# Optimization experiments

Measured on AMD Instinct MI355X. Metric: run time of the kernel, lower is better.

The kernel has to match this reference:

```python
import jax, jax.numpy as jnp
import numpy as np

B, Cin, Cout, T, H, W = 8, 64, 64, 16, 32, 32
AH = 64  # attention_hidden_dims


def setup_inputs() -> dict:
    key = jax.random.key(0)
    ks = jax.random.split(key, 6)
    s = 0.05
    return {
        "X": jax.random.normal(ks[0], (B, Cin, T, H, W), jnp.float32),
        # 1x1 conv weights of the SelfAttention module (bias zero-init like nn.Conv2d default is uniform, but zeros is fine for a reference baseline)
        "q_w": jax.random.normal(ks[1], (AH, Cin), jnp.float32) * s,
        "q_b": jnp.zeros((AH,), jnp.float32),
        "k_w": jax.random.normal(ks[2], (AH, Cin), jnp.float32) * s,
        "k_b": jnp.zeros((AH,), jnp.float32),
        "v_w": jax.random.normal(ks[3], (Cin, Cin), jnp.float32) * s,
        "v_b": jnp.zeros((Cin,), jnp.float32),
        # ConvLSTM gate conv: concat([x, h]) -> 4*Cout channels, 3x3, padding 1
        "conv_w": jax.random.normal(ks[4], (4 * Cout, Cin + Cout, 3, 3), jnp.float32) * s,
        "conv_b": jnp.zeros((4 * Cout,), jnp.float32),
        # peephole weights, zero-init per WeightsInitializer.Zeros
        "w_ci": jnp.zeros((Cout, H, W), jnp.float32),
        "w_cf": jnp.zeros((Cout, H, W), jnp.float32),
        "w_co": jnp.zeros((Cout, H, W), jnp.float32),
    }


def _self_attention(x, q_w, q_b, k_w, k_b, v_w, v_b):
    # x: (B, Cin, H, W). 1x1 convs expressed as channel contractions.
    b, c, h, w = x.shape
    xf = x.reshape(b, c, h * w)                                    # (B, C, HW)
    q = jnp.einsum('oc,bcn->bno', q_w, xf) + q_b                   # (B, HW, AH)
    k = jnp.einsum('oc,bcn->bon', k_w, xf) + k_b[None, :, None]    # (B, AH, HW)
    v = jnp.einsum('oc,bcn->bon', v_w, xf) + v_b[None, :, None]    # (B, Cin, HW)
    attn = jax.nn.softmax(jnp.einsum('bno,bom->bnm', q, k), axis=-1)  # (B, HW, HW)
    out = jnp.einsum('bnm,bcm->bcn', attn, v).reshape(b, c, h, w)  # (B, Cin, H, W)
    return out, attn


def _convlstm_cell(x, h, c, conv_w, conv_b, w_ci, w_cf, w_co):
    z = jnp.concatenate([x, h], axis=1)  # (B, Cin+Cout, H, W)
    conv = jax.lax.conv_general_dilated(
        z, conv_w, window_strides=(1, 1), padding='SAME',
        dimension_numbers=('NCHW', 'OIHW', 'NCHW')) + conv_b[None, :, None, None]
    i_c, f_c, g_c, o_c = jnp.split(conv, 4, axis=1)
    i = jax.nn.sigmoid(i_c + w_ci * c)
    f = jax.nn.sigmoid(f_c + w_cf * c)
    new_c = f * c + i * jnp.tanh(g_c)
    o = jax.nn.sigmoid(o_c + w_co * new_c)
    new_h = o * jnp.tanh(new_c)
    return new_h, new_c


def reference(X, q_w, q_b, k_w, k_b, v_w, v_b, conv_w, conv_b, w_ci, w_cf, w_co):
    b = X.shape[0]
    h0 = jnp.zeros((b, Cout, H, W), X.dtype)
    c0 = jnp.zeros_like(h0)
    xs = jnp.moveaxis(X, 2, 0)  # (T, B, Cin, H, W) for scan over time

    def step(carry, x_t):
        h, c = carry
        ax, _ = _self_attention(x_t, q_w, q_b, k_w, k_b, v_w, v_b)
        new_h, new_c = _convlstm_cell(ax, h, c, conv_w, conv_b, w_ci, w_cf, w_co)
        return (new_h, new_c), new_h

    _, hs = jax.lax.scan(step, (h0, c0), xs)  # hs: (T, B, Cout, H, W)
    return jnp.moveaxis(hs, 0, 2)  # (B, Cout, T, H, W)
```

## Files before the change

### kernel.cpp

```cpp
#include <hip/hip_runtime.h>
#include <math.h>

typedef __attribute__((ext_vector_type(8))) __bf16 bf16x8;
typedef __attribute__((ext_vector_type(4))) float f32x4;
typedef unsigned short u16;
typedef unsigned int u32;

#define MFMA16(a, b, c) __builtin_amdgcn_mfma_f32_16x16x32_bf16(a, b, c, 0, 0, 0)

__device__ __forceinline__ u16 f2bf(float f) {
    u32 u = __float_as_uint(f);
    return (u16)((u + 0x7fffu + ((u >> 16) & 1u)) >> 16);
}
__device__ __forceinline__ float bf2f(u16 h) {
    return __uint_as_float(((u32)h) << 16);
}

__global__ __launch_bounds__(256) void k_wtrans2(const float* __restrict__ cw,
                                                 u16* __restrict__ whi,
                                                 u16* __restrict__ wlo) {
    int idx = blockIdx.x * 256 + threadIdx.x;
    if (idx >= 294912) return;
    int s   = idx >> 15;
    int ocp = (idx >> 7) & 255;
    int ic  = idx & 127;
    int q = ocp >> 5, cc = (ocp >> 2) & 7, g = ocp & 3;
    int oc = g * 64 + q * 8 + cc;
    float f = cw[oc * 1152 + ic * 9 + s];
    u16 hi = f2bf(f);
    whi[idx] = hi;
    wlo[idx] = f2bf(f - bf2f(hi));
}

__global__ __launch_bounds__(256) void k_qkvw(
    const float* __restrict__ qw, const float* __restrict__ kw,
    const float* __restrict__ vw, u16* __restrict__ w2h, u16* __restrict__ w2l)
{
    int idx = blockIdx.x * 256 + threadIdx.x;
    if (idx >= 12288) return;
    int o = idx >> 6, c = idx & 63;
    float f = (o < 64) ? qw[o * 64 + c]
            : (o < 128) ? kw[(o - 64) * 64 + c]
                        : vw[(o - 128) * 64 + c];
    u16 hi = f2bf(f);
    w2h[idx] = hi;
    w2l[idx] = f2bf(f - bf2f(hi));
}

__global__ __launch_bounds__(256) void k_qkv2(
    const float* __restrict__ X,
    const u16* __restrict__ w2h, const u16* __restrict__ w2l,
    const float* __restrict__ qb, const float* __restrict__ kb,
    const float* __restrict__ vb,
    u16* __restrict__ qmat, u16* __restrict__ kmat, u16* __restrict__ vt)
{
    __shared__ u16 bhs[4096];
    __shared__ u16 bls[4096];

    const int tid = threadIdx.x;
    const int ns = blockIdx.x;
    const int bt = blockIdx.y;
    const int b = bt >> 4, t = bt & 15;
    const int n0 = ns * 64;

    const float* xb = X + (size_t)b * 1048576 + (size_t)t * 1024 + n0;
    for (int i = tid; i < 4096; i += 256) {
        int c = i >> 6, n = i & 63;
        float f = xb[(size_t)c * 16384 + n];
        u16 hi = f2bf(f);
        u16 lo = f2bf(f - bf2f(hi));
        int ci = c ^ ((n & 7) << 3);
        bhs[n * 64 + ci] = hi;
        bls[n * 64 + ci] = lo;
    }
    __syncthreads();

    const int wv = tid >> 6, lane = tid & 63;
    const int l15 = lane & 15, l4 = lane >> 4;
    const int o0 = wv * 48;

    f32x4 acc[3][4];
#pragma unroll
    for (int ot = 0; ot < 3; ++ot)
#pragma unroll
        for (int nt = 0; nt < 4; ++nt) acc[ot][nt] = (f32x4){0.f, 0.f, 0.f, 0.f};

#pragma unroll
    for (int kk = 0; kk < 2; ++kk) {
        bf16x8 Ah[3], Al[3];
#pragma unroll
        for (int ot = 0; ot < 3; ++ot) {
            int off = (o0 + ot * 16 + l15) * 64 + kk * 32 + l4 * 8;
            Ah[ot] = *reinterpret_cast<const bf16x8*>(w2h + off);
            Al[ot] = *reinterpret_cast<const bf16x8*>(w2l + off);
        }
#pragma unroll
        for (int nt = 0; nt < 4; ++nt) {
            int n = nt * 16 + l15;
            int gran = (kk * 4 + l4) ^ (n & 7);
            bf16x8 Bh = *reinterpret_cast<const bf16x8*>(bhs + n * 64 + gran * 8);
            bf16x8 Bl = *reinterpret_cast<const bf16x8*>(bls + n * 64 + gran * 8);
#pragma unroll
            for (int ot = 0; ot < 3; ++ot) {
                acc[ot][nt] = MFMA16(Ah[ot], Bh, acc[ot][nt]);
                acc[ot][nt] = MFMA16(Ah[ot], Bl, acc[ot][nt]);
                acc[ot][nt] = MFMA16(Al[ot], Bh, acc[ot][nt]);
            }
        }
    }

#pragma unroll
    for (int ot = 0; ot < 3; ++ot) {
#pragma unroll
        for (int r = 0; r < 4; ++r) {
            int row = o0 + ot * 16 + l4 * 4 + r;
            float bias = (row < 64) ? qb[row]
                       : (row < 128) ? kb[row - 64] : vb[row - 128];
#pragma unroll
            for (int nt = 0; nt < 4; ++nt) {
                int col = n0 + nt * 16 + l15;
                u16 h = f2bf(acc[ot][nt][r] + bias);
                if (row < 64)
                    qmat[(size_t)bt * 65536 + (size_t)col * 64 + row] = h;
                else if (row < 128)
                    kmat[(size_t)bt * 65536 + (size_t)col * 64 + (row - 64)] = h;
                else
                    vt[(size_t)bt * 65536 + (size_t)(row - 128) * 1024 + col] = h;
            }
        }
    }
}

__global__ __launch_bounds__(512, 2) void k_attn2(
    const u16* __restrict__ qmat, const u16* __restrict__ kmat,
    const u16* __restrict__ vt, u16* __restrict__ za)
{
    __shared__ char kl[16384];
    __shared__ char vl[16384];
    __shared__ u16 plds[8 * 16 * 40];

    const int tid = threadIdx.x;
    const int id  = blockIdx.x;
    const int w   = (id & 7) * 128 + (id >> 3);
    const int bt  = w >> 3;
    const int nt8 = w & 7;

    const int wv = tid >> 6, lane = tid & 63;
    const int l15 = lane & 15, l4 = lane >> 4;
    const int n0 = nt8 * 128 + wv * 16;

    const u16* qb_ = qmat + (size_t)bt * 65536;
    const u16* kb_ = kmat + (size_t)bt * 65536;
    const u16* vb_ = vt + (size_t)bt * 65536;
    u16* zab = za + (size_t)bt * 147968;

    if (nt8 == 0) {
        for (int j = tid; j < 2112; j += 512) {
            int pi = j >> 4, q16 = j & 15;
            int px = (pi < 34) ? pi
                   : (pi < 68) ? (33 * 34 + (pi - 34))
                               : ((1 + ((pi - 68) >> 1)) * 34 + ((pi - 68) & 1) * 33);
            *reinterpret_cast<uint4*>(zab + px * 128 + q16 * 8) =
                make_uint4(0u, 0u, 0u, 0u);
        }
    }

    bf16x8 qf0 = *reinterpret_cast<const bf16x8*>(qb_ + (n0 + l15) * 64 + l4 * 8);
    bf16x8 qf1 = *reinterpret_cast<const bf16x8*>(qb_ + (n0 + l15) * 64 + 32 + l4 * 8);

    f32x4 oacc[4];
#pragma unroll
    for (int ct = 0; ct < 4; ++ct) oacc[ct] = (f32x4){0.f, 0.f, 0.f, 0.f};
    float lsum = 0.f;
    char* plc = (char*)plds + wv * 1280;

    bf16x8 kst[2], vst[2];
#pragma unroll
    for (int r = 0; r < 2; ++r) {
        int c = tid + r * 512;
        kst[r] = *reinterpret_cast<const bf16x8*>(kb_ + (c >> 3) * 64 + (c & 7) * 8);
        vst[r] = *reinterpret_cast<const bf16x8*>(vb_ + (c >> 4) * 1024 + (c & 15) * 8);
    }

    for (int mt = 0; mt < 8; ++mt) {
        __syncthreads();
#pragma unroll
        for (int r = 0; r < 2; ++r) {
            int c = tid + r * 512;
            int m = c >> 3, sl = c & 7;
            *reinterpret_cast<bf16x8*>(kl + ((m * 128 + sl * 16) ^ ((m & 7) << 4))) = kst[r];
            int cc = c >> 4, sl2 = c & 15;
            *reinterpret_cast<bf16x8*>(vl + ((cc * 256 + sl2 * 16) ^ ((cc & 7) << 4))) = vst[r];
        }
        __syncthreads();
        if (mt < 7) {
            int mg = (mt + 1) * 128;
#pragma unroll
            for (int r = 0; r < 2; ++r) {
                int c = tid + r * 512;
                kst[r] = *reinterpret_cast<const bf16x8*>(kb_ + (mg + (c >> 3)) * 64 + (c & 7) * 8);
                vst[r] = *reinterpret_cast<const bf16x8*>(vb_ + (c >> 4) * 1024 + mg + (c & 15) * 8);
            }
        }

#pragma unroll
        for (int mi2 = 0; mi2 < 4; ++mi2) {
#pragma unroll
            for (int hf = 0; hf < 2; ++hf) {
                int ml = (mi2 * 2 + hf) * 16 + l15;
                f32x4 s = {0.f, 0.f, 0.f, 0.f};
                bf16x8 ka0 = *reinterpret_cast<const bf16x8*>(
                    kl + ((ml * 128 + l4 * 16) ^ ((ml & 7) << 4)));
                bf16x8 ka1 = *reinterpret_cast<const bf16x8*>(
                    kl + ((ml * 128 + 64 + l4 * 16) ^ ((ml & 7) << 4)));
                s = MFMA16(ka0, qf0, s);
                s = MFMA16(ka1, qf1, s);
                float p0 = __expf(s[0]);
                float p1 = __expf(s[1]);
                float p2 = __expf(s[2]);
                float p3 = __expf(s[3]);
                lsum += (p0 + p1) + (p2 + p3);
                u32 pa = (u32)f2bf(p0) | ((u32)f2bf(p1) << 16);
                u32 pb = (u32)f2bf(p2) | ((u32)f2bf(p3) << 16);
                *reinterpret_cast<uint2*>(plc + l15 * 80 + hf * 32 + l4 * 8) =
                    make_uint2(pa, pb);
            }
            bf16x8 pfrag = *reinterpret_cast<const bf16x8*>(plc + l15 * 80 + l4 * 16);
#pragma unroll
            for (int ct = 0; ct < 4; ++ct) {
                bf16x8 vfrag = *reinterpret_cast<const bf16x8*>(
                    vl + (((ct * 16 + l15) * 256 + mi2 * 64 + l4 * 16) ^ ((l15 & 7) << 4)));
                oacc[ct] = MFMA16(pfrag, vfrag, oacc[ct]);
            }
        }
    }

    lsum += __shfl_xor(lsum, 16, 64);
    lsum += __shfl_xor(lsum, 32, 64);

#pragma unroll
    for (int r = 0; r < 4; ++r) {
        float linv = 1.f / __shfl(lsum, l4 * 4 + r, 64);
        int nrow = n0 + l4 * 4 + r;
        u16* base = zab + (((nrow >> 5) + 1) * 34 + (nrow & 31) + 1) * 128;
#pragma unroll
        for (int ct = 0; ct < 4; ++ct) {
            float v = oacc[ct][r] * linv;
            u16 hi = f2bf(v);
            base[ct * 16 + l15]      = hi;
            base[64 + ct * 16 + l15] = f2bf(v - bf2f(hi));
        }
    }
}

__global__ __launch_bounds__(256) void k_cell4(
    const u16* __restrict__ za, const u16* __restrict__ zh_in,
    u16* __restrict__ zh_out, float* __restrict__ cst,
    const u16* __restrict__ whi, const u16* __restrict__ wlo,
    const float* __restrict__ conv_b,
    const float* __restrict__ wci, const float* __restrict__ wcf,
    const float* __restrict__ wco, float* __restrict__ out, int t)
{
    __shared__ __align__(16) char zt[17408];

    const int tid = threadIdx.x;
    const int id  = blockIdx.x;
    const int w   = (id & 7) * 64 + (id >> 3);
    const int b   = w >> 6;
    const int oq  = (w >> 4) & 3;
    const int ys  = w & 15;
    const int y0  = ys * 2;
    const int bt  = b * 16 + t;

    const int wv = tid >> 6, lane = tid & 63;
    const int l15 = lane & 15, l4 = lane >> 4;
    const int ow = wv & 1, pw = wv >> 1;

    const u16* zab = za + (size_t)bt * 147968;
    const u16* zhb = zh_in + (size_t)b * 147968;

    f32x4 acc[2][2];
#pragma unroll
    for (int sub = 0; sub < 2; ++sub)
#pragma unroll
        for (int nt = 0; nt < 2; ++nt) acc[sub][nt] = (f32x4){0.f, 0.f, 0.f, 0.f};

    for (int ck = 0; ck < 4; ++ck) {
        const u16* src = (ck < 2) ? zab : zhb;
        const int c0 = (ck & 1) * 32;
        __syncthreads();
        for (int g = tid; g < 1088; g += 256) {
            int p = g >> 3, slot = g & 7;
            int ly = p / 34, col = p - ly * 34;
            int gp = (y0 + ly) * 34 + col;
            int soff = (slot < 4) ? (c0 + slot * 8) : (64 + c0 + (slot - 4) * 8);
            uint4 v = *reinterpret_cast<const uint4*>(src + gp * 128 + soff);
            *reinterpret_cast<uint4*>(zt + p * 128 + ((slot * 16) ^ ((p & 7) << 4))) = v;
        }
        __syncthreads();

#pragma unroll
        for (int s = 0; s < 9; ++s) {
            const int dy = s / 3 - 1, dx = s % 3 - 1;
            bf16x8 Ah[2], Al[2];
#pragma unroll
            for (int sub = 0; sub < 2; ++sub) {
                size_t woff = (size_t)(s * 256 + oq * 64 + ow * 32 + sub * 16 + l15) * 128
                              + ck * 32 + l4 * 8;
                Ah[sub] = *reinterpret_cast<const bf16x8*>(whi + woff);
                Al[sub] = *reinterpret_cast<const bf16x8*>(wlo + woff);
            }
#pragma unroll
            for (int nt = 0; nt < 2; ++nt) {
                int pxl = (pw + dy + 1) * 34 + nt * 16 + l15 + 1 + dx;
                int swz = (pxl & 7) << 4;
                bf16x8 Bh = *reinterpret_cast<const bf16x8*>(
                    zt + pxl * 128 + ((l4 * 16) ^ swz));
                bf16x8 Bl = *reinterpret_cast<const bf16x8*>(
                    zt + pxl * 128 + ((64 + l4 * 16) ^ swz));
#pragma unroll
                for (int sub = 0; sub < 2; ++sub) {
                    acc[sub][nt] = MFMA16(Ah[sub], Bh, acc[sub][nt]);
                    acc[sub][nt] = MFMA16(Ah[sub], Bl, acc[sub][nt]);
                    acc[sub][nt] = MFMA16(Al[sub], Bh, acc[sub][nt]);
                }
            }
        }
    }

    u16* zho = zh_out + (size_t)b * 147968;
    const int chq = (oq * 2 + ow) * 8;
    const int y = y0 + pw;
#pragma unroll
    for (int sub = 0; sub < 2; ++sub) {
        int ch = chq + sub * 4 + l4;
        float bi = conv_b[ch], bf = conv_b[64 + ch];
        float bg = conv_b[128 + ch], bo = conv_b[192 + ch];
#pragma unroll
        for (int nt = 0; nt < 2; ++nt) {
            int x = nt * 16 + l15;
            int n = y * 32 + x;
            float ci = acc[sub][nt][0] + bi;
            float cf = acc[sub][nt][1] + bf;
            float cg = acc[sub][nt][2] + bg;
            float co = acc[sub][nt][3] + bo;
            size_t si = ((size_t)b * 64 + ch) * 1024 + n;
            int pw_ = ch * 1024 + n;
            float cp = cst[si];
            float iv = 1.f / (1.f + __expf(-(ci + wci[pw_] * cp)));
            float fv = 1.f / (1.f + __expf(-(cf + wcf[pw_] * cp)));
            float nc = fv * cp + iv * tanhf(cg);
            float ov = 1.f / (1.f + __expf(-(co + wco[pw_] * nc)));
            float nh = ov * tanhf(nc);
            cst[si] = nc;
            out[(((size_t)b * 64 + ch) * 16 + t) * 1024 + n] = nh;
            u16 hhi = f2bf(nh);
            u16* zp = zho + ((y + 1) * 34 + (x + 1)) * 128;
            zp[ch]      = hhi;
            zp[64 + ch] = f2bf(nh - bf2f(hhi));
        }
    }
}

#define OB_Q    0ull
#define OB_K    16777216ull
#define OB_V    33554432ull
#define OB_ZA   50331648ull
#define OB_ZH0  88211456ull
#define OB_ZH1  90578944ull
#define OB_CST  92946432ull
#define OB_WHI  95043584ull
#define OB_WLO  95633408ull
#define OB_WQ2H 96223232ull
#define OB_WQ2L 96247808ull

extern "C" void kernel_launch(void* const* d_in, const int* in_sizes, int n_in,
                              void* d_out, int out_size, void* d_ws, size_t ws_size,
                              hipStream_t stream)
{
    const float* X   = (const float*)d_in[0];
    const float* qw  = (const float*)d_in[1];
    const float* qb  = (const float*)d_in[2];
    const float* kw  = (const float*)d_in[3];
    const float* kb  = (const float*)d_in[4];
    const float* vw  = (const float*)d_in[5];
    const float* vb  = (const float*)d_in[6];
    const float* cw  = (const float*)d_in[7];
    const float* cb  = (const float*)d_in[8];
    const float* wci = (const float*)d_in[9];
    const float* wcf = (const float*)d_in[10];
    const float* wco = (const float*)d_in[11];
    float* out = (float*)d_out;
    char* wsb  = (char*)d_ws;

    u16* qmat = (u16*)(wsb + OB_Q);
    u16* kmat = (u16*)(wsb + OB_K);
    u16* vt   = (u16*)(wsb + OB_V);
    u16* za   = (u16*)(wsb + OB_ZA);
    u16* zh0  = (u16*)(wsb + OB_ZH0);
    u16* zh1  = (u16*)(wsb + OB_ZH1);
    float* cst= (float*)(wsb + OB_CST);
    u16* whi  = (u16*)(wsb + OB_WHI);
    u16* wlo  = (u16*)(wsb + OB_WLO);
    u16* w2h  = (u16*)(wsb + OB_WQ2H);
    u16* w2l  = (u16*)(wsb + OB_WQ2L);

    hipMemsetAsync(zh0, 0, 6832128ull, stream);
    k_wtrans2<<<1152, 256, 0, stream>>>(cw, whi, wlo);
    k_qkvw<<<48, 256, 0, stream>>>(qw, kw, vw, w2h, w2l);
    k_qkv2<<<dim3(16, 128), 256, 0, stream>>>(X, w2h, w2l, qb, kb, vb,
                                              qmat, kmat, vt);
    k_attn2<<<1024, 512, 0, stream>>>(qmat, kmat, vt, za);

    for (int t = 0; t < 16; ++t) {
        u16* hin  = (t & 1) ? zh1 : zh0;
        u16* hout = (t & 1) ? zh0 : zh1;
        k_cell4<<<512, 256, 0, stream>>>(za, hin, hout, cst, whi, wlo,
                                         cb, wci, wcf, wco, out, t);
    }
}
```

Baseline: 740.1 us.

## Double the ConvLSTM cell tile to four rows and register-prefetch next input chunk

Each block of the ConvLSTM cell kernel now handles four output rows with 512 threads instead of two rows with 256, which cuts the redundant halo rows loaded per block and halves the grid. The global-to-shared staging is now software-pipelined: the next channel chunk is loaded into registers while MFMAs on the current chunk run, and the per-thread staging addresses are computed once up front. This uses more registers and more shared memory per block, which may lower occupancy. With only 256 blocks there may also be less parallelism across the GPU.

Result: slower. 828.1 us (+11.9%).

```diff
diff --git a/kernel.cpp b/kernel.cpp
--- a/kernel.cpp
+++ b/kernel.cpp
@@ -253,7 +253,7 @@
     }
 }
 
-__global__ __launch_bounds__(256) void k_cell4(
+__global__ __launch_bounds__(512) void k_cell5(
     const u16* __restrict__ za, const u16* __restrict__ zh_in,
     u16* __restrict__ zh_out, float* __restrict__ cst,
     const u16* __restrict__ whi, const u16* __restrict__ wlo,
@@ -261,15 +261,15 @@
     const float* __restrict__ wci, const float* __restrict__ wcf,
     const float* __restrict__ wco, float* __restrict__ out, int t)
 {
-    __shared__ __align__(16) char zt[17408];
+    __shared__ __align__(16) char zt[26112];
 
     const int tid = threadIdx.x;
     const int id  = blockIdx.x;
-    const int w   = (id & 7) * 64 + (id >> 3);
-    const int b   = w >> 6;
-    const int oq  = (w >> 4) & 3;
-    const int ys  = w & 15;
-    const int y0  = ys * 2;
+    const int w   = (id & 7) * 32 + (id >> 3);
+    const int b   = w >> 5;
+    const int oq  = (w >> 3) & 3;
+    const int ys  = w & 7;
+    const int y0  = ys * 4;
     const int bt  = b * 16 + t;
 
     const int wv = tid >> 6, lane = tid & 63;
@@ -279,25 +279,45 @@
     const u16* zab = za + (size_t)bt * 147968;
     const u16* zhb = zh_in + (size_t)b * 147968;
 
+    int gp_[4], sb_[4], lo_[4];
+    const int ng = (tid < 96) ? 4 : 3;
+#pragma unroll
+    for (int r = 0; r < 4; ++r) {
+        int g = tid + r * 512;
+        if (g >= 1632) g = 0;
+        int p = g >> 3, slot = g & 7;
+        int ly = p / 34, col = p - ly * 34;
+        gp_[r] = (y0 + ly) * 34 + col;
+        sb_[r] = (slot < 4) ? slot * 8 : 64 + (slot - 4) * 8;
+        lo_[r] = p * 128 + ((slot * 16) ^ ((p & 7) << 4));
+    }
+
     f32x4 acc[2][2];
 #pragma unroll
     for (int sub = 0; sub < 2; ++sub)
 #pragma unroll
         for (int nt = 0; nt < 2; ++nt) acc[sub][nt] = (f32x4){0.f, 0.f, 0.f, 0.f};
 
+    uint4 st[4];
+#pragma unroll
+    for (int r = 0; r < 4; ++r)
+        if (r < ng)
+            st[r] = *reinterpret_cast<const uint4*>(zab + gp_[r] * 128 + sb_[r]);
+
     for (int ck = 0; ck < 4; ++ck) {
-        const u16* src = (ck < 2) ? zab : zhb;
-        const int c0 = (ck & 1) * 32;
         __syncthreads();
-        for (int g = tid; g < 1088; g += 256) {
-            int p = g >> 3, slot = g & 7;
-            int ly = p / 34, col = p - ly * 34;
-            int gp = (y0 + ly) * 34 + col;
-            int soff = (slot < 4) ? (c0 + slot * 8) : (64 + c0 + (slot - 4) * 8);
-            uint4 v = *reinterpret_cast<const uint4*>(src + gp * 128 + soff);
-            *reinterpret_cast<uint4*>(zt + p * 128 + ((slot * 16) ^ ((p & 7) << 4))) = v;
-        }
+#pragma unroll
+        for (int r = 0; r < 4; ++r)
+            if (r < ng) *reinterpret_cast<uint4*>(zt + lo_[r]) = st[r];
         __syncthreads();
+        if (ck < 3) {
+            const u16* src = (ck + 1 < 2) ? zab : zhb;
+            const int c0 = ((ck + 1) & 1) * 32;
+#pragma unroll
+            for (int r = 0; r < 4; ++r)
+                if (r < ng)
+                    st[r] = *reinterpret_cast<const uint4*>(src + gp_[r] * 128 + sb_[r] + c0);
+        }
 
 #pragma unroll
         for (int s = 0; s < 9; ++s) {
@@ -415,7 +435,7 @@
     for (int t = 0; t < 16; ++t) {
         u16* hin  = (t & 1) ? zh1 : zh0;
         u16* hout = (t & 1) ? zh0 : zh1;
-        k_cell4<<<512, 256, 0, stream>>>(za, hin, hout, cst, whi, wlo,
+        k_cell5<<<256, 512, 0, stream>>>(za, hin, hout, cst, whi, wlo,
                                          cb, wci, wcf, wco, out, t);
     }
 }
```
